# Optimization experiments

Hardware: AMD Instinct MI355X
Metric: run time of the kernel (lower is better)

The kernel has to match this reference:

```python
import jax, jax.numpy as jnp
import numpy as np

B, L, D, H = 2, 2048, 1024, 16
HD = D // H
HID = 4 * D
EPS = 1e-5


def setup_inputs() -> dict:
    key = jax.random.key(0)
    ks = jax.random.split(key, 16)
    s = 0.02
    inp = {
        "x": jax.random.normal(ks[0], (B, L, D), jnp.float32),
        "mask": jnp.triu(jnp.ones((L, L), bool), k=1),  # True above diagonal -> masked
        "wq": jax.random.normal(ks[1], (D, D), jnp.float32) * s,
        "wk": jax.random.normal(ks[2], (D, D), jnp.float32) * s,
        "wv": jax.random.normal(ks[3], (D, D), jnp.float32) * s,
        "wo": jax.random.normal(ks[4], (D, D), jnp.float32) * s,
        "ln1_g": jnp.ones((D,), jnp.float32),
        "ln1_b": jnp.zeros((D,), jnp.float32),
        "ln2_g": jnp.ones((D,), jnp.float32),
        "ln2_b": jnp.zeros((D,), jnp.float32),
        "w1": jax.random.normal(ks[5], (HID, D), jnp.float32) * s,
        "b1": jnp.zeros((HID,), jnp.float32),
        "wg": jax.random.normal(ks[6], (HID, D), jnp.float32) * s,
        "w2": jax.random.normal(ks[7], (D, HID), jnp.float32) * s,
        "b2": jnp.zeros((D,), jnp.float32),
    }
    return inp


def _layernorm(x, g, b):
    mu = jnp.mean(x, axis=-1, keepdims=True)
    var = jnp.mean(jnp.square(x - mu), axis=-1, keepdims=True)
    return (x - mu) * jax.lax.rsqrt(var + EPS) * g + b


def _attention(h, mask, wq, wk, wv, wo):
    b, l, d = h.shape
    scale = HD ** -0.5
    # torch Linear: y = x @ W.T (W is [out, in])
    q = (h @ wq.T).reshape(b, l, H, HD)
    k = (h @ wk.T).reshape(b, l, H, HD)
    v = (h @ wv.T).reshape(b, l, H, HD)
    attn = jnp.einsum("bqhd,bkhd->bhqk", q, k) * scale
    attn = jnp.where(mask[None, None, :, :], -jnp.inf, attn)
    pos_bias = jnp.arange(l, dtype=attn.dtype) * 0.01  # additive bias along key axis
    attn = attn + pos_bias[None, None, None, :]
    attn = jax.nn.softmax(attn, axis=-1)
    out = jnp.einsum("bhqk,bkhd->bqhd", attn, v).reshape(b, l, d)
    return out @ wo.T


def _ffn(h, w1, b1, wg, w2, b2):
    return (jax.nn.silu(h @ w1.T + b1) * (h @ wg.T)) @ w2.T + b2


def reference(x, mask, wq, wk, wv, wo, ln1_g, ln1_b, ln2_g, ln2_b, w1, b1, wg, w2, b2):
    x = x + _attention(_layernorm(x, ln1_g, ln1_b), mask, wq, wk, wv, wo)
    x = x + _ffn(_layernorm(x, ln2_g, ln2_b), w1, b1, wg, w2, b2)
    return x
```

## Files before the change

kernel.cpp:

```cpp
#include <hip/hip_runtime.h>

#define ML   2048
#define MD   1024
#define MH   16
#define MHD  64
#define MB   2
#define MM   4096
#define MHID 4096

typedef unsigned short u16;
typedef short bf16x8 __attribute__((ext_vector_type(8)));
typedef float f32x4 __attribute__((ext_vector_type(4)));

__device__ __forceinline__ u16 f2bf(float f) {
    union { float f; unsigned u; } c; c.f = f;
    unsigned r = c.u + 0x7fffu + ((c.u >> 16) & 1u);
    return (u16)(r >> 16);
}
__device__ __forceinline__ float bf2f(u16 h) {
    union { unsigned u; float f; } c; c.u = ((unsigned)h) << 16;
    return c.f;
}

__device__ __forceinline__ void async_copy16(const u16* g, u16* l) {
    __builtin_amdgcn_global_load_lds(
        (const __attribute__((address_space(1))) void*)g,
        (__attribute__((address_space(3))) void*)l, 16, 0, 0);
}

struct ConvPack {
    const float* src[13];
    u16* dst[13];
    int n[13];
    int start[14];
};

__global__ __launch_bounds__(256)
void conv_all(ConvPack p)
{
    const int bx = blockIdx.x;
    int seg = 0;
    while (seg < 12 && bx >= p.start[seg + 1]) ++seg;
    const int local = bx - p.start[seg];
    const int idx = (local * 256 + threadIdx.x) * 8;
    if (idx >= p.n[seg]) return;
    const float* in = p.src[seg];
    const float4 a = *(const float4*)(in + idx);
    const float4 b = *(const float4*)(in + idx + 4);
    union { bf16x8 v; u16 s[8]; } u;
    u.s[0] = f2bf(a.x); u.s[1] = f2bf(a.y); u.s[2] = f2bf(a.z); u.s[3] = f2bf(a.w);
    u.s[4] = f2bf(b.x); u.s[5] = f2bf(b.y); u.s[6] = f2bf(b.z); u.s[7] = f2bf(b.w);
    *(bf16x8*)&p.dst[seg][idx] = u.v;
}

template<int MI, int NI>
__device__ __forceinline__ void gemm_core(
    const u16* __restrict__ A, const u16* __restrict__ Bm,
    int m0, int n0, int lda, int ldb, int K,
    u16* As, u16* Bs, f32x4 (&acc)[MI][NI])
{
    constexpr int TM = MI * 32;
    constexpr int TN = NI * 32;
    const int tid  = threadIdx.x;
    const int wave = tid >> 6, lane = tid & 63;
    const int wm = wave & 1, wn = wave >> 1;
    const int l15 = lane & 15, quad = lane >> 4;

    const int srow = wave * 16 + (lane >> 2);
    const int scol = (lane & 3) * 8;
    const u16* Ag = A  + (size_t)(m0 + srow) * lda + scol;
    const u16* Bg = Bm + (size_t)(n0 + srow) * ldb + scol;
    u16* Asw = As + srow * 32 + scol;
    u16* Bsw = Bs + srow * 32 + scol;

    f32x4 zero4 = {0.f, 0.f, 0.f, 0.f};
#pragma unroll
    for (int mi = 0; mi < MI; ++mi)
#pragma unroll
        for (int ni = 0; ni < NI; ++ni) acc[mi][ni] = zero4;

    for (int k0 = 0; k0 < K; k0 += 32) {
        __syncthreads();
#pragma unroll
        for (int p = 0; p < TM / 64; ++p)
            async_copy16(Ag + k0 + (size_t)p * 64 * lda, Asw + p * 64 * 32);
#pragma unroll
        for (int p = 0; p < TN / 64; ++p)
            async_copy16(Bg + k0 + (size_t)p * 64 * ldb, Bsw + p * 64 * 32);
        __syncthreads();

        bf16x8 af[MI], bfr[NI];
#pragma unroll
        for (int mi = 0; mi < MI; ++mi)
            af[mi] = *(const bf16x8*)&As[(wm * MI * 16 + mi * 16 + l15) * 32 + quad * 8];
#pragma unroll
        for (int ni = 0; ni < NI; ++ni)
            bfr[ni] = *(const bf16x8*)&Bs[(wn * NI * 16 + ni * 16 + l15) * 32 + quad * 8];
#pragma unroll
        for (int mi = 0; mi < MI; ++mi)
#pragma unroll
            for (int ni = 0; ni < NI; ++ni)
                acc[mi][ni] = __builtin_amdgcn_mfma_f32_16x16x32_bf16(
                    af[mi], bfr[ni], acc[mi][ni], 0, 0, 0);
    }
}

__global__ __launch_bounds__(256)
void ln_kernel(const float* __restrict__ xin,
               const u16* __restrict__ g, const u16* __restrict__ bb,
               u16* __restrict__ out,
               const u16* __restrict__ rbias, float* __restrict__ oinit)
{
    const int row = blockIdx.x;
    const int tid = threadIdx.x;
    const float4 t = *(const float4*)(xin + (size_t)row * MD + tid * 4);
    float v[4] = {t.x, t.y, t.z, t.w};
    if (oinit) {
        const ushort4 rb = *(const ushort4*)&rbias[tid * 4];
        float4 oi;
        oi.x = v[0] + bf2f(rb.x);
        oi.y = v[1] + bf2f(rb.y);
        oi.z = v[2] + bf2f(rb.z);
        oi.w = v[3] + bf2f(rb.w);
        *(float4*)&oinit[(size_t)row * MD + tid * 4] = oi;
    }
    float s  = v[0] + v[1] + v[2] + v[3];
    float s2 = v[0]*v[0] + v[1]*v[1] + v[2]*v[2] + v[3]*v[3];
#pragma unroll
    for (int off = 1; off < 64; off <<= 1) {
        s  += __shfl_xor(s,  off);
        s2 += __shfl_xor(s2, off);
    }
    __shared__ float red[8];
    const int wave = tid >> 6, lane = tid & 63;
    if (lane == 0) { red[wave] = s; red[4 + wave] = s2; }
    __syncthreads();
    s  = red[0] + red[1] + red[2] + red[3];
    s2 = red[4] + red[5] + red[6] + red[7];
    const float mu  = s * (1.0f / MD);
    const float var = fmaxf(s2 * (1.0f / MD) - mu * mu, 0.0f);
    const float rs  = rsqrtf(var + 1e-5f);
    const ushort4 gv = *(const ushort4*)&g[tid * 4];
    const ushort4 bv = *(const ushort4*)&bb[tid * 4];
    ushort4 o;
    o.x = f2bf((v[0] - mu) * rs * bf2f(gv.x) + bf2f(bv.x));
    o.y = f2bf((v[1] - mu) * rs * bf2f(gv.y) + bf2f(bv.y));
    o.z = f2bf((v[2] - mu) * rs * bf2f(gv.z) + bf2f(bv.z));
    o.w = f2bf((v[3] - mu) * rs * bf2f(gv.w) + bf2f(bv.w));
    *(ushort4*)&out[(size_t)row * MD + tid * 4] = o;
}

__global__ __launch_bounds__(256, 2)
void gemm_qkv(const u16* __restrict__ ln, const u16* __restrict__ wq,
              const u16* __restrict__ wk, const u16* __restrict__ wv,
              u16* __restrict__ q, u16* __restrict__ k, u16* __restrict__ vt)
{
    __shared__ __align__(16) u16 As[128 * 32];
    __shared__ __align__(16) u16 Bs[128 * 32];
    const int z = blockIdx.z;
    const u16* Bm = (z == 0) ? wq : (z == 1) ? wk : wv;
    const int m0 = blockIdx.x * 128, n0 = blockIdx.y * 128;
    f32x4 acc[4][4];
    gemm_core<4, 4>(ln, Bm, m0, n0, MD, MD, MD, As, Bs, acc);

    const int tid = threadIdx.x;
    const int wave = tid >> 6, lane = tid & 63;
    const int wm = wave & 1, wn = wave >> 1, l15 = lane & 15, quad = lane >> 4;
    if (z < 2) {
        u16* out = (z == 0) ? q : k;
        const float scale = (z == 0) ? 0.125f : 1.0f;
#pragma unroll
        for (int mi = 0; mi < 4; ++mi)
#pragma unroll
            for (int ni = 0; ni < 4; ++ni)
#pragma unroll
                for (int r = 0; r < 4; ++r) {
                    const int row = m0 + wm * 64 + mi * 16 + quad * 4 + r;
                    const int col = n0 + wn * 64 + ni * 16 + l15;
                    out[(size_t)row * MD + col] = f2bf(acc[mi][ni][r] * scale);
                }
    } else {
#pragma unroll
        for (int mi = 0; mi < 4; ++mi)
#pragma unroll
            for (int ni = 0; ni < 4; ++ni) {
                const int row0 = m0 + wm * 64 + mi * 16 + quad * 4;
                const int col  = n0 + wn * 64 + ni * 16 + l15;
                const int bb = row0 >> 11, l = row0 & (ML - 1);
                const int hh = col >> 6,  hd = col & (MHD - 1);
                ushort4 pk;
                pk.x = f2bf(acc[mi][ni][0]);
                pk.y = f2bf(acc[mi][ni][1]);
                pk.z = f2bf(acc[mi][ni][2]);
                pk.w = f2bf(acc[mi][ni][3]);
                *(ushort4*)&vt[((size_t)(bb * MH + hh) * MHD + hd) * ML + l] = pk;
            }
    }
}

__global__ __launch_bounds__(256, 2)
void attn_kernel(const u16* __restrict__ Q, const u16* __restrict__ Kb,
                 const u16* __restrict__ Vt, u16* __restrict__ O)
{
    __shared__ __align__(16) u16 Ks[64 * 64];
    __shared__ __align__(16) u16 Vs[64 * 64];
    __shared__ __align__(16) u16 Pl[4][16 * 72];
    const int tid = threadIdx.x, wave = tid >> 6, lane = tid & 63;
    const int quad = lane >> 4, l15 = lane & 15;
    const int idx = blockIdx.x;
    const int qt = (ML / 64 - 1) - (idx >> 5);
    const int hb = idx & 31;
    const int h = hb & 15, b = hb >> 4;
    const int q0 = qt * 64;
    const int qrow = q0 + wave * 16;
    const float L2E = 1.44269504f;
    const float C1 = 0.01f * L2E;
    const float C2 = -32.0f * L2E;

    u16* Plw = Pl[wave];

    const size_t qoff = ((size_t)(b * ML + qrow + l15)) * MD + h * MHD + quad * 8;
    const bf16x8 aq0 = *(const bf16x8*)&Q[qoff];
    const bf16x8 aq1 = *(const bf16x8*)&Q[qoff + 32];

    const int str = tid >> 3;
    const int sj  = tid & 7;
    const int sjx = (sj ^ (str & 7)) * 8;
    const u16* Kg = Kb + (size_t)(b * ML) * MD + h * MHD;
    const u16* Vg = Vt + (size_t)((b * MH + h) * MHD) * ML;

    const int rsw0 = ((quad    ) ^ (l15 & 7)) * 8;
    const int rsw1 = ((quad + 4) ^ (l15 & 7)) * 8;

    bf16x8 onesf;
    {
        const short v = (l15 == 0) ? (short)0x3F80 : (short)0;
        onesf = (bf16x8){v, v, v, v, v, v, v, v};
    }

    f32x4 zero4 = {0.f, 0.f, 0.f, 0.f};
    f32x4 Oacc[4];
    f32x4 lsum = zero4;
#pragma unroll
    for (int i = 0; i < 4; ++i) Oacc[i] = zero4;

    for (int kt = 0; kt <= qt; ++kt) {
        const int k0 = kt * 64;

        __syncthreads();
        async_copy16(Kg + (size_t)(k0 + str) * MD + sjx,        Ks + tid * 8);
        async_copy16(Kg + (size_t)(k0 + 32 + str) * MD + sjx,   Ks + 2048 + tid * 8);
        async_copy16(Vg + (size_t)str * ML + k0 + sjx,          Vs + tid * 8);
        async_copy16(Vg + (size_t)(32 + str) * ML + k0 + sjx,   Vs + 2048 + tid * 8);
        __syncthreads();

        f32x4 s[4];
#pragma unroll
        for (int jn = 0; jn < 4; ++jn) {
            const int krow = (jn * 16 + l15) * 64;
            const bf16x8 k0f = *(const bf16x8*)&Ks[krow + rsw0];
            const bf16x8 k1f = *(const bf16x8*)&Ks[krow + rsw1];
            f32x4 z = zero4;
            z = __builtin_amdgcn_mfma_f32_16x16x32_bf16(aq0, k0f, z, 0, 0, 0);
            z = __builtin_amdgcn_mfma_f32_16x16x32_bf16(aq1, k1f, z, 0, 0, 0);
            s[jn] = z;
        }

        const bool diag = (kt == qt);
#pragma unroll
        for (int jn = 0; jn < 4; ++jn) {
            const int key = k0 + jn * 16 + l15;
            const float pbm = fmaf((float)key, C1, C2);
#pragma unroll
            for (int r = 0; r < 4; ++r) {
                float val = fmaf(s[jn][r], L2E, pbm);
                if (diag && key > qrow + quad * 4 + r) val = -30000.f;
                union { float f; unsigned u; } c;
                c.f = exp2f(val);
                Plw[(quad * 4 + r) * 72 + jn * 16 + l15] = (u16)(c.u >> 16);
            }
        }

        bf16x8 vv[4][2];
#pragma unroll
        for (int j = 0; j < 4; ++j) {
            const int vrow = (j * 16 + l15) * 64;
            vv[j][0] = *(const bf16x8*)&Vs[vrow + rsw0];
            vv[j][1] = *(const bf16x8*)&Vs[vrow + rsw1];
        }

        const bf16x8 ap0 = *(const bf16x8*)&Plw[l15 * 72 + quad * 8];
        const bf16x8 ap1 = *(const bf16x8*)&Plw[l15 * 72 + 32 + quad * 8];
#pragma unroll
        for (int j = 0; j < 4; ++j) {
            Oacc[j] = __builtin_amdgcn_mfma_f32_16x16x32_bf16(ap0, vv[j][0], Oacc[j], 0, 0, 0);
            Oacc[j] = __builtin_amdgcn_mfma_f32_16x16x32_bf16(ap1, vv[j][1], Oacc[j], 0, 0, 0);
        }
        lsum = __builtin_amdgcn_mfma_f32_16x16x32_bf16(ap0, onesf, lsum, 0, 0, 0);
        lsum = __builtin_amdgcn_mfma_f32_16x16x32_bf16(ap1, onesf, lsum, 0, 0, 0);
    }

#pragma unroll
    for (int r = 0; r < 4; ++r) {
        const float l = __shfl(lsum[r], lane & 48);
        const float inv = 1.0f / l;
        const int row = qrow + quad * 4 + r;
#pragma unroll
        for (int j = 0; j < 4; ++j) {
            const int col = h * MHD + j * 16 + l15;
            O[((size_t)(b * ML + row)) * MD + col] = f2bf(Oacc[j][r] * inv);
        }
    }
}

__global__ __launch_bounds__(256, 2)
void gemm_wo(const u16* __restrict__ ao, const u16* __restrict__ wo,
             const float* __restrict__ x, float* __restrict__ h1)
{
    __shared__ __align__(16) u16 As[64 * 32];
    __shared__ __align__(16) u16 Bs[128 * 32];
    const int m0 = blockIdx.x * 64, n0 = blockIdx.y * 128;
    f32x4 acc[2][4];
    gemm_core<2, 4>(ao, wo, m0, n0, MD, MD, MD, As, Bs, acc);
    const int tid = threadIdx.x;
    const int wave = tid >> 6, lane = tid & 63;
    const int wm = wave & 1, wn = wave >> 1, l15 = lane & 15, quad = lane >> 4;
#pragma unroll
    for (int mi = 0; mi < 2; ++mi)
#pragma unroll
        for (int ni = 0; ni < 4; ++ni)
#pragma unroll
            for (int r = 0; r < 4; ++r) {
                const int row = m0 + wm * 32 + mi * 16 + quad * 4 + r;
                const int col = n0 + wn * 64 + ni * 16 + l15;
                const size_t idx = (size_t)row * MD + col;
                h1[idx] = acc[mi][ni][r] + x[idx];
            }
}

__global__ __launch_bounds__(512, 2)
void gemm_ug256(const u16* __restrict__ ln, const u16* __restrict__ w1,
                const u16* __restrict__ wg, const u16* __restrict__ b1,
                u16* __restrict__ hf)
{
    __shared__ __align__(16) u16 smem[4][16384];
    const int tid = threadIdx.x;
    const int wave = tid >> 6, lane = tid & 63;
    const int wm = wave >> 2, wn = wave & 3;
    const int l15 = lane & 15, quad = lane >> 4;
    const int m0 = blockIdx.x * 256, n0 = blockIdx.y * 128;

    const int str = tid >> 3;
    const int sjx = ((tid & 7) ^ (str & 7)) * 8;
    const u16* Ag  = ln + (size_t)(m0 + str) * MD + sjx;
    const u16* B1g = w1 + (size_t)(n0 + str) * MD + sjx;
    const u16* B2g = wg + (size_t)(n0 + str) * MD + sjx;

    f32x4 zero4 = {0.f, 0.f, 0.f, 0.f};
    f32x4 acc[8][4];
#pragma unroll
    for (int mi = 0; mi < 8; ++mi)
#pragma unroll
        for (int ni = 0; ni < 4; ++ni) acc[mi][ni] = zero4;

#define UG_STAGE(d, k0)                                                        \
    do {                                                                       \
        _Pragma("unroll")                                                      \
        for (int p = 0; p < 4; ++p)                                            \
            async_copy16(Ag + (size_t)p * 64 * MD + (k0),                      \
                         &smem[d][p * 4096 + tid * 8]);                        \
        _Pragma("unroll")                                                      \
        for (int p = 0; p < 2; ++p)                                            \
            async_copy16(B1g + (size_t)p * 64 * MD + (k0),                     \
                         &smem[2 + (d)][p * 4096 + tid * 8]);                  \
        _Pragma("unroll")                                                      \
        for (int p = 0; p < 2; ++p)                                            \
            async_copy16(B2g + (size_t)p * 64 * MD + (k0),                     \
                         &smem[2 + (d)][(p + 2) * 4096 + tid * 8]);            \
    } while (0)

    UG_STAGE(0, 0);
    __syncthreads();

    for (int t = 0; t < 16; ++t) {
        const int d = t & 1;
        const u16* Abuf = smem[d];
        const u16* Bbuf = smem[2 + d];

        bf16x8 bfr[4][2], af0[4][2];
#pragma unroll
        for (int ni = 0; ni < 4; ++ni)
#pragma unroll
            for (int kh = 0; kh < 2; ++kh)
                bfr[ni][kh] = *(const bf16x8*)&Bbuf[(wn * 64 + ni * 16 + l15) * 64
                                                    + ((kh * 4 + quad) ^ (l15 & 7)) * 8];
#pragma unroll
        for (int mi = 0; mi < 4; ++mi)
#pragma unroll
            for (int kh = 0; kh < 2; ++kh)
                af0[mi][kh] = *(const bf16x8*)&Abuf[(wm * 128 + mi * 16 + l15) * 64
                                                    + ((kh * 4 + quad) ^ (l15 & 7)) * 8];

        if (t < 15) UG_STAGE(d ^ 1, (t + 1) * 64);

        __builtin_amdgcn_s_setprio(1);
#pragma unroll
        for (int mi = 0; mi < 4; ++mi)
#pragma unroll
            for (int ni = 0; ni < 4; ++ni) {
                acc[mi][ni] = __builtin_amdgcn_mfma_f32_16x16x32_bf16(
                    af0[mi][0], bfr[ni][0], acc[mi][ni], 0, 0, 0);
                acc[mi][ni] = __builtin_amdgcn_mfma_f32_16x16x32_bf16(
                    af0[mi][1], bfr[ni][1], acc[mi][ni], 0, 0, 0);
            }
        __builtin_amdgcn_s_setprio(0);
        __builtin_amdgcn_s_barrier();

        bf16x8 af1[4][2];
#pragma unroll
        for (int mi = 0; mi < 4; ++mi)
#pragma unroll
            for (int kh = 0; kh < 2; ++kh)
                af1[mi][kh] = *(const bf16x8*)&Abuf[(wm * 128 + (mi + 4) * 16 + l15) * 64
                                                    + ((kh * 4 + quad) ^ (l15 & 7)) * 8];
        __builtin_amdgcn_s_setprio(1);
#pragma unroll
        for (int mi = 0; mi < 4; ++mi)
#pragma unroll
            for (int ni = 0; ni < 4; ++ni) {
                acc[mi + 4][ni] = __builtin_amdgcn_mfma_f32_16x16x32_bf16(
                    af1[mi][0], bfr[ni][0], acc[mi + 4][ni], 0, 0, 0);
                acc[mi + 4][ni] = __builtin_amdgcn_mfma_f32_16x16x32_bf16(
                    af1[mi][1], bfr[ni][1], acc[mi + 4][ni], 0, 0, 0);
            }
        __builtin_amdgcn_s_setprio(0);

        __syncthreads();
    }
#undef UG_STAGE

    float* X = (float*)&smem[0][0];
    if (wn < 2) {
        float* Xw = X + (wm * 2 + wn) * 8192;
#pragma unroll
        for (int mi = 0; mi < 8; ++mi)
#pragma unroll
            for (int ni = 0; ni < 4; ++ni)
#pragma unroll
                for (int r = 0; r < 4; ++r)
                    Xw[((mi * 4 + ni) * 4 + r) * 64 + lane] = acc[mi][ni][r];
    }
    __syncthreads();
    if (wn >= 2) {
        const float* Xw = X + (wm * 2 + (wn - 2)) * 8192;
#pragma unroll
        for (int mi = 0; mi < 8; ++mi)
#pragma unroll
            for (int ni = 0; ni < 4; ++ni) {
                const int col = n0 + (wn - 2) * 64 + ni * 16 + l15;
                const float bb1 = bf2f(b1[col]);
#pragma unroll
                for (int r = 0; r < 4; ++r) {
                    const int row = m0 + wm * 128 + mi * 16 + quad * 4 + r;
                    const float uv = Xw[((mi * 4 + ni) * 4 + r) * 64 + lane] + bb1;
                    const float si = uv / (1.0f + __expf(-uv));
                    hf[(size_t)row * MHID + col] = f2bf(si * acc[mi][ni][r]);
                }
            }
    }
}

__global__ __launch_bounds__(256, 2)
void gemm_w2(const u16* __restrict__ hf, const u16* __restrict__ w2,
             float* __restrict__ out)
{
    __shared__ __align__(16) u16 As[128 * 32];
    __shared__ __align__(16) u16 Bs[128 * 32];
    const int m0 = blockIdx.x * 128, n0 = blockIdx.y * 128;
    const int kz = blockIdx.z * 2048;
    f32x4 acc[4][4];
    gemm_core<4, 4>(hf + kz, w2 + kz, m0, n0, MHID, MHID, 2048, As, Bs, acc);
    const int tid = threadIdx.x;
    const int wave = tid >> 6, lane = tid & 63;
    const int wm = wave & 1, wn = wave >> 1, l15 = lane & 15, quad = lane >> 4;
#pragma unroll
    for (int mi = 0; mi < 4; ++mi)
#pragma unroll
        for (int ni = 0; ni < 4; ++ni)
#pragma unroll
            for (int r = 0; r < 4; ++r) {
                const int row = m0 + wm * 64 + mi * 16 + quad * 4 + r;
                const int col = n0 + wn * 64 + ni * 16 + l15;
                unsafeAtomicAdd(&out[(size_t)row * MD + col], acc[mi][ni][r]);
            }
}

extern "C" void kernel_launch(void* const* d_in, const int* in_sizes, int n_in,
                              void* d_out, int out_size, void* d_ws, size_t ws_size,
                              hipStream_t stream)
{
    const float* x    = (const float*)d_in[0];
    const float* wq   = (const float*)d_in[2];
    const float* wk   = (const float*)d_in[3];
    const float* wv   = (const float*)d_in[4];
    const float* wo   = (const float*)d_in[5];
    const float* ln1g = (const float*)d_in[6];
    const float* ln1b = (const float*)d_in[7];
    const float* ln2g = (const float*)d_in[8];
    const float* ln2b = (const float*)d_in[9];
    const float* w1   = (const float*)d_in[10];
    const float* b1   = (const float*)d_in[11];
    const float* wgp  = (const float*)d_in[12];
    const float* w2   = (const float*)d_in[13];
    const float* b2   = (const float*)d_in[14];
    float* out = (float*)d_out;

    char* ws = (char*)d_ws;
    u16*  wqb  = (u16*)(ws);
    u16*  wkb  = (u16*)(ws + ((size_t)2  << 20));
    u16*  wvb  = (u16*)(ws + ((size_t)4  << 20));
    u16*  wob  = (u16*)(ws + ((size_t)6  << 20));
    u16*  w1b  = (u16*)(ws + ((size_t)8  << 20));
    u16*  wgb  = (u16*)(ws + ((size_t)16 << 20));
    u16*  w2b  = (u16*)(ws + ((size_t)24 << 20));
    char* vec  = ws + ((size_t)32 << 20);
    u16*  l1g  = (u16*)(vec);
    u16*  l1b  = (u16*)(vec + 4096);
    u16*  l2g  = (u16*)(vec + 8192);
    u16*  l2b  = (u16*)(vec + 12288);
    u16*  b1b  = (u16*)(vec + 16384);
    u16*  b2b  = (u16*)(vec + 24576);
    u16*   ln  = (u16*)(ws + ((size_t)33 << 20));
    u16*   q   = (u16*)(ws + ((size_t)41 << 20));
    u16*   k   = (u16*)(ws + ((size_t)49 << 20));
    u16*   vt  = (u16*)(ws + ((size_t)57 << 20));
    u16*   ao  = ln;
    float* h1  = (float*)(ws + ((size_t)41 << 20));
    u16*   hf  = (u16*)(ws + ((size_t)89 << 20));

    const int NW = MD * MD;
    const int NF = MHID * MD;
    ConvPack cp;
    const float* srcs[13] = {wq, wk, wv, wo, w1, wgp, w2, ln1g, ln1b, ln2g, ln2b, b1, b2};
    u16* dsts[13]         = {wqb, wkb, wvb, wob, w1b, wgb, w2b, l1g, l1b, l2g, l2b, b1b, b2b};
    int  ns[13]           = {NW, NW, NW, NW, NF, NF, NF, MD, MD, MD, MD, MHID, MD};
    int start = 0;
    for (int i = 0; i < 13; ++i) {
        cp.src[i] = srcs[i]; cp.dst[i] = dsts[i]; cp.n[i] = ns[i];
        cp.start[i] = start;
        start += (ns[i] + 2047) / 2048;
    }
    cp.start[13] = start;
    conv_all<<<start, 256, 0, stream>>>(cp);

    ln_kernel<<<MM, 256, 0, stream>>>(x, l1g, l1b, ln, nullptr, nullptr);
    gemm_qkv<<<dim3(MM / 128, MD / 128, 3), 256, 0, stream>>>(ln, wqb, wkb, wvb, q, k, vt);
    attn_kernel<<<(ML / 64) * MH * MB, 256, 0, stream>>>(q, k, vt, ao);
    gemm_wo<<<dim3(MM / 64, MD / 128), 256, 0, stream>>>(ao, wob, x, h1);
    ln_kernel<<<MM, 256, 0, stream>>>(h1, l2g, l2b, ln, b2b, out);
    gemm_ug256<<<dim3(MM / 256, MHID / 128), 512, 0, stream>>>(ln, w1b, wgb, b1b, hf);
    gemm_w2<<<dim3(MM / 128, MD / 128, 2), 256, 0, stream>>>(hf, w2b, out);
}
```

Baseline: 408.3 us.

## Process two query tiles per attention block and split w2 GEMM into four K-slices

The attention kernel now handles 128 query rows per block as two 64-row halves that share each loaded K/V tile, so K/V shared-memory staging is amortized over twice the queries. The grid is halved and each wave keeps two sets of accumulators, which raises register pressure. Separately, the final FFN GEMM splits K into four slices instead of two, giving more blocks for parallelism at the cost of more atomic adds into the output.

After: 454.5 us. 11.3% more time.

```diff
diff --git a/kernel.cpp b/kernel.cpp
--- a/kernel.cpp
+++ b/kernel.cpp
@@ -208,20 +208,24 @@
     const int tid = threadIdx.x, wave = tid >> 6, lane = tid & 63;
     const int quad = lane >> 4, l15 = lane & 15;
     const int idx = blockIdx.x;
-    const int qt = (ML / 64 - 1) - (idx >> 5);
+    const int qt = (ML / 128 - 1) - (idx >> 5);
     const int hb = idx & 31;
     const int h = hb & 15, b = hb >> 4;
-    const int q0 = qt * 64;
-    const int qrow = q0 + wave * 16;
+    const int q0 = qt * 128;
+    const int rowA = q0 + wave * 16;
+    const int rowB = q0 + 64 + wave * 16;
     const float L2E = 1.44269504f;
     const float C1 = 0.01f * L2E;
     const float C2 = -32.0f * L2E;
 
     u16* Plw = Pl[wave];
 
-    const size_t qoff = ((size_t)(b * ML + qrow + l15)) * MD + h * MHD + quad * 8;
-    const bf16x8 aq0 = *(const bf16x8*)&Q[qoff];
-    const bf16x8 aq1 = *(const bf16x8*)&Q[qoff + 32];
+    const size_t qoffA = ((size_t)(b * ML + rowA + l15)) * MD + h * MHD + quad * 8;
+    const bf16x8 aqA0 = *(const bf16x8*)&Q[qoffA];
+    const bf16x8 aqA1 = *(const bf16x8*)&Q[qoffA + 32];
+    const size_t qoffB = qoffA + (size_t)64 * MD;
+    const bf16x8 aqB0 = *(const bf16x8*)&Q[qoffB];
+    const bf16x8 aqB1 = *(const bf16x8*)&Q[qoffB + 32];
 
     const int str = tid >> 3;
     const int sj  = tid & 7;
@@ -239,12 +243,13 @@
     }
 
     f32x4 zero4 = {0.f, 0.f, 0.f, 0.f};
-    f32x4 Oacc[4];
-    f32x4 lsum = zero4;
-#pragma unroll
-    for (int i = 0; i < 4; ++i) Oacc[i] = zero4;
-
-    for (int kt = 0; kt <= qt; ++kt) {
+    f32x4 OaccA[4], OaccB[4];
+    f32x4 lsumA = zero4, lsumB = zero4;
+#pragma unroll
+    for (int i = 0; i < 4; ++i) { OaccA[i] = zero4; OaccB[i] = zero4; }
+
+    const int ktmax = 2 * qt + 1;
+    for (int kt = 0; kt <= ktmax; ++kt) {
         const int k0 = kt * 64;
 
         __syncthreads();
@@ -254,61 +259,108 @@
         async_copy16(Vg + (size_t)(32 + str) * ML + k0 + sjx,   Vs + 2048 + tid * 8);
         __syncthreads();
 
-        f32x4 s[4];
-#pragma unroll
-        for (int jn = 0; jn < 4; ++jn) {
-            const int krow = (jn * 16 + l15) * 64;
-            const bf16x8 k0f = *(const bf16x8*)&Ks[krow + rsw0];
-            const bf16x8 k1f = *(const bf16x8*)&Ks[krow + rsw1];
-            f32x4 z = zero4;
-            z = __builtin_amdgcn_mfma_f32_16x16x32_bf16(aq0, k0f, z, 0, 0, 0);
-            z = __builtin_amdgcn_mfma_f32_16x16x32_bf16(aq1, k1f, z, 0, 0, 0);
-            s[jn] = z;
+        if (kt <= 2 * qt) {
+            f32x4 s[4];
+#pragma unroll
+            for (int jn = 0; jn < 4; ++jn) {
+                const int krow = (jn * 16 + l15) * 64;
+                const bf16x8 k0f = *(const bf16x8*)&Ks[krow + rsw0];
+                const bf16x8 k1f = *(const bf16x8*)&Ks[krow + rsw1];
+                f32x4 z = zero4;
+                z = __builtin_amdgcn_mfma_f32_16x16x32_bf16(aqA0, k0f, z, 0, 0, 0);
+                z = __builtin_amdgcn_mfma_f32_16x16x32_bf16(aqA1, k1f, z, 0, 0, 0);
+                s[jn] = z;
+            }
+            const bool diag = (kt == 2 * qt);
+#pragma unroll
+            for (int jn = 0; jn < 4; ++jn) {
+                const int key = k0 + jn * 16 + l15;
+                const float pbm = fmaf((float)key, C1, C2);
+#pragma unroll
+                for (int r = 0; r < 4; ++r) {
+                    float val = fmaf(s[jn][r], L2E, pbm);
+                    if (diag && key > rowA + quad * 4 + r) val = -30000.f;
+                    union { float f; unsigned u; } c;
+                    c.f = exp2f(val);
+                    Plw[(quad * 4 + r) * 72 + jn * 16 + l15] = (u16)(c.u >> 16);
+                }
+            }
+            bf16x8 vv[4][2];
+#pragma unroll
+            for (int j = 0; j < 4; ++j) {
+                const int vrow = (j * 16 + l15) * 64;
+                vv[j][0] = *(const bf16x8*)&Vs[vrow + rsw0];
+                vv[j][1] = *(const bf16x8*)&Vs[vrow + rsw1];
+            }
+            const bf16x8 ap0 = *(const bf16x8*)&Plw[l15 * 72 + quad * 8];
+            const bf16x8 ap1 = *(const bf16x8*)&Plw[l15 * 72 + 32 + quad * 8];
+#pragma unroll
+            for (int j = 0; j < 4; ++j) {
+                OaccA[j] = __builtin_amdgcn_mfma_f32_16x16x32_bf16(ap0, vv[j][0], OaccA[j], 0, 0, 0);
+                OaccA[j] = __builtin_amdgcn_mfma_f32_16x16x32_bf16(ap1, vv[j][1], OaccA[j], 0, 0, 0);
+            }
+            lsumA = __builtin_amdgcn_mfma_f32_16x16x32_bf16(ap0, onesf, lsumA, 0, 0, 0);
+            lsumA = __builtin_amdgcn_mfma_f32_16x16x32_bf16(ap1, onesf, lsumA, 0, 0, 0);
         }
 
-        const bool diag = (kt == qt);
-#pragma unroll
-        for (int jn = 0; jn < 4; ++jn) {
-            const int key = k0 + jn * 16 + l15;
-            const float pbm = fmaf((float)key, C1, C2);
-#pragma unroll
-            for (int r = 0; r < 4; ++r) {
-                float val = fmaf(s[jn][r], L2E, pbm);
-                if (diag && key > qrow + quad * 4 + r) val = -30000.f;
-                union { float f; unsigned u; } c;
-                c.f = exp2f(val);
-                Plw[(quad * 4 + r) * 72 + jn * 16 + l15] = (u16)(c.u >> 16);
-            }
+        {
+            f32x4 s[4];
+#pragma unroll
+            for (int jn = 0; jn < 4; ++jn) {
+                const int krow = (jn * 16 + l15) * 64;
+                const bf16x8 k0f = *(const bf16x8*)&Ks[krow + rsw0];
+                const bf16x8 k1f = *(const bf16x8*)&Ks[krow + rsw1];
+                f32x4 z = zero4;
+                z = __builtin_amdgcn_mfma_f32_16x16x32_bf16(aqB0, k0f, z, 0, 0, 0);
+                z = __builtin_amdgcn_mfma_f32_16x16x32_bf16(aqB1, k1f, z, 0, 0, 0);
+                s[jn] = z;
+            }
+            const bool diag = (kt == ktmax);
+#pragma unroll
+            for (int jn = 0; jn < 4; ++jn) {
+                const int key = k0 + jn * 16 + l15;
+                const float pbm = fmaf((float)key, C1, C2);
+#pragma unroll
+                for (int r = 0; r < 4; ++r) {
+                    float val = fmaf(s[jn][r], L2E, pbm);
+                    if (diag && key > rowB + quad * 4 + r) val = -30000.f;
+                    union { float f; unsigned u; } c;
+                    c.f = exp2f(val);
+                    Plw[(quad * 4 + r) * 72 + jn * 16 + l15] = (u16)(c.u >> 16);
+                }
+            }
+            bf16x8 vv[4][2];
+#pragma unroll
+            for (int j = 0; j < 4; ++j) {
+                const int vrow = (j * 16 + l15) * 64;
+                vv[j][0] = *(const bf16x8*)&Vs[vrow + rsw0];
+                vv[j][1] = *(const bf16x8*)&Vs[vrow + rsw1];
+            }
+            const bf16x8 ap0 = *(const bf16x8*)&Plw[l15 * 72 + quad * 8];
+            const bf16x8 ap1 = *(const bf16x8*)&Plw[l15 * 72 + 32 + quad * 8];
+#pragma unroll
+            for (int j = 0; j < 4; ++j) {
+                OaccB[j] = __builtin_amdgcn_mfma_f32_16x16x32_bf16(ap0, vv[j][0], OaccB[j], 0, 0, 0);
+                OaccB[j] = __builtin_amdgcn_mfma_f32_16x16x32_bf16(ap1, vv[j][1], OaccB[j], 0, 0, 0);
+            }
+            lsumB = __builtin_amdgcn_mfma_f32_16x16x32_bf16(ap0, onesf, lsumB, 0, 0, 0);
+            lsumB = __builtin_amdgcn_mfma_f32_16x16x32_bf16(ap1, onesf, lsumB, 0, 0, 0);
         }
-
-        bf16x8 vv[4][2];
-#pragma unroll
-        for (int j = 0; j < 4; ++j) {
-            const int vrow = (j * 16 + l15) * 64;
-            vv[j][0] = *(const bf16x8*)&Vs[vrow + rsw0];
-            vv[j][1] = *(const bf16x8*)&Vs[vrow + rsw1];
-        }
-
-        const bf16x8 ap0 = *(const bf16x8*)&Plw[l15 * 72 + quad * 8];
-        const bf16x8 ap1 = *(const bf16x8*)&Plw[l15 * 72 + 32 + quad * 8];
-#pragma unroll
-        for (int j = 0; j < 4; ++j) {
-            Oacc[j] = __builtin_amdgcn_mfma_f32_16x16x32_bf16(ap0, vv[j][0], Oacc[j], 0, 0, 0);
-            Oacc[j] = __builtin_amdgcn_mfma_f32_16x16x32_bf16(ap1, vv[j][1], Oacc[j], 0, 0, 0);
-        }
-        lsum = __builtin_amdgcn_mfma_f32_16x16x32_bf16(ap0, onesf, lsum, 0, 0, 0);
-        lsum = __builtin_amdgcn_mfma_f32_16x16x32_bf16(ap1, onesf, lsum, 0, 0, 0);
     }
 
 #pragma unroll
     for (int r = 0; r < 4; ++r) {
-        const float l = __shfl(lsum[r], lane & 48);
-        const float inv = 1.0f / l;
-        const int row = qrow + quad * 4 + r;
+        const float la = __shfl(lsumA[r], lane & 48);
+        const float lb = __shfl(lsumB[r], lane & 48);
+        const float invA = 1.0f / la;
+        const float invB = 1.0f / lb;
+        const int ra = rowA + quad * 4 + r;
+        const int rb = rowB + quad * 4 + r;
 #pragma unroll
         for (int j = 0; j < 4; ++j) {
             const int col = h * MHD + j * 16 + l15;
-            O[((size_t)(b * ML + row)) * MD + col] = f2bf(Oacc[j][r] * inv);
+            O[((size_t)(b * ML + ra)) * MD + col] = f2bf(OaccA[j][r] * invA);
+            O[((size_t)(b * ML + rb)) * MD + col] = f2bf(OaccB[j][r] * invB);
         }
     }
 }
@@ -477,9 +529,9 @@
     __shared__ __align__(16) u16 As[128 * 32];
     __shared__ __align__(16) u16 Bs[128 * 32];
     const int m0 = blockIdx.x * 128, n0 = blockIdx.y * 128;
-    const int kz = blockIdx.z * 2048;
+    const int kz = blockIdx.z * 1024;
     f32x4 acc[4][4];
-    gemm_core<4, 4>(hf + kz, w2 + kz, m0, n0, MHID, MHID, 2048, As, Bs, acc);
+    gemm_core<4, 4>(hf + kz, w2 + kz, m0, n0, MHID, MHID, 1024, As, Bs, acc);
     const int tid = threadIdx.x;
     const int wave = tid >> 6, lane = tid & 63;
     const int wm = wave & 1, wn = wave >> 1, l15 = lane & 15, quad = lane >> 4;
@@ -555,9 +607,9 @@
 
     ln_kernel<<<MM, 256, 0, stream>>>(x, l1g, l1b, ln, nullptr, nullptr);
     gemm_qkv<<<dim3(MM / 128, MD / 128, 3), 256, 0, stream>>>(ln, wqb, wkb, wvb, q, k, vt);
-    attn_kernel<<<(ML / 64) * MH * MB, 256, 0, stream>>>(q, k, vt, ao);
+    attn_kernel<<<(ML / 128) * MH * MB, 256, 0, stream>>>(q, k, vt, ao);
     gemm_wo<<<dim3(MM / 64, MD / 128), 256, 0, stream>>>(ao, wob, x, h1);
     ln_kernel<<<MM, 256, 0, stream>>>(h1, l2g, l2b, ln, b2b, out);
     gemm_ug256<<<dim3(MM / 256, MHID / 128), 512, 0, stream>>>(ln, w1b, wgb, b1b, hf);
-    gemm_w2<<<dim3(MM / 128, MD / 128, 2), 256, 0, stream>>>(hf, w2b, out);
-}
+    gemm_w2<<<dim3(MM / 128, MD / 128, 4), 256, 0, stream>>>(hf, w2b, out);
+}
```
